# Kernel optimization log

Hardware: AMD Instinct MI355X
Metric: run time of the kernel (lower is better)

The kernel has to match this reference:

```python
import jax, jax.numpy as jnp
import numpy as np

N_NODES = 100000


def _gcn_conv(x, W, b, src, dst, dinv):
    # PyG GCNConv: h = X @ W; out[i] = sum_{j->i} norm_ji * h[j] (incl. self-loop); + b
    h = x @ W                                   # [N, F_out]
    norm = dinv[src] * dinv[dst]                # [E]
    agg = jax.ops.segment_sum(norm[:, None] * h[src], dst, num_segments=N_NODES)
    agg = agg + (dinv * dinv)[:, None] * h      # self-loop contribution
    return agg + b


def setup_inputs() -> dict:
    key = jax.random.key(0)
    ks = jax.random.split(key, 12)
    N, E, F = N_NODES, 3200000, 128

    def glorot(k, fan_in, fan_out):
        s = float(np.sqrt(6.0 / (fan_in + fan_out)))
        return jax.random.uniform(k, (fan_in, fan_out), jnp.float32, -s, s)

    x = jax.random.normal(ks[0], (N, F), jnp.float32)
    edge_index = jax.random.randint(ks[1], (2, E), 0, N, jnp.int64)
    return {
        "x": x,
        "edge_index": edge_index,
        "W1": glorot(ks[2], F, 64),  "b1": jnp.zeros((64,), jnp.float32),
        "W2": glorot(ks[3], 64, 32), "b2": jnp.zeros((32,), jnp.float32),
        "W3": glorot(ks[4], 32, 16), "b3": jnp.zeros((16,), jnp.float32),
        "Ws02": glorot(ks[5], F, 32),  "bs02": jnp.zeros((32,), jnp.float32),
        "Ws03": glorot(ks[6], F, 16),  "bs03": jnp.zeros((16,), jnp.float32),
        "Ws13": glorot(ks[7], 64, 16), "bs13": jnp.zeros((16,), jnp.float32),
    }


def reference(x, edge_index, W1, b1, W2, b2, W3, b3, Ws02, bs02, Ws03, bs03, Ws13, bs13):
    src, dst = edge_index[0], edge_index[1]
    # symmetric GCN normalization with self-loops: deg[i] = 1 + in-degree(i)
    deg = jax.ops.segment_sum(jnp.ones_like(dst, dtype=x.dtype), dst, num_segments=N_NODES) + 1.0
    dinv = jax.lax.rsqrt(deg)

    # eval-mode: dropout is identity
    x1 = jax.nn.relu(_gcn_conv(x, W1, b1, src, dst, dinv))            # [N, 64]
    x2 = jax.nn.relu(_gcn_conv(x1, W2, b2, src, dst, dinv)) + (x @ Ws02 + bs02)   # [N, 32]
    x3 = (jax.nn.relu(_gcn_conv(x2, W3, b3, src, dst, dinv))
          + (x @ Ws03 + bs03) + (x1 @ Ws13 + bs13))                   # [N, 16]
    return x3
```

## Files before the change

kernel.cpp:

```cpp
#include <hip/hip_runtime.h>

#define NN 100000
#define NB 256
#define NPB 391
#define MSCH 4096

__device__ inline unsigned short f2bf(float f) {
    unsigned u = __float_as_uint(f);
    return (unsigned short)((u + 0x7FFFu + ((u >> 16) & 1u)) >> 16);
}
__device__ inline unsigned packbf(float a, float b) {
    return (unsigned)f2bf(a) | ((unsigned)f2bf(b) << 16);
}
__device__ inline float bflo(unsigned u) { return __uint_as_float(u << 16); }
__device__ inline float bfhi(unsigned u) { return __uint_as_float(u & 0xFFFF0000u); }
__device__ inline float4 bf4(uint2 u) {
    return make_float4(bflo(u.x), bfhi(u.x), bflo(u.y), bfhi(u.y));
}

__device__ inline void fp8acc(unsigned u, float4& a) {
    auto lo = __builtin_amdgcn_cvt_pk_f32_fp8((int)u, false);
    auto hi = __builtin_amdgcn_cvt_pk_f32_fp8((int)u, true);
    a.x += lo[0]; a.y += lo[1]; a.z += hi[0]; a.w += hi[1];
}
__device__ inline unsigned char f2fp8(float v) {
    return (unsigned char)(__builtin_amdgcn_cvt_pk_fp8_f32(v, 0.f, 0, false) & 0xFF);
}
__device__ inline unsigned short f2fp8x2(float a, float b) {
    return (unsigned short)(__builtin_amdgcn_cvt_pk_fp8_f32(a, b, 0, false) & 0xFFFF);
}

typedef __attribute__((ext_vector_type(8))) short bf16x8;
typedef __attribute__((ext_vector_type(4))) float f32x4;


__global__ __launch_bounds__(256) void histA_kernel(const int* __restrict__ dst, int E,
                                                    int* __restrict__ counts) {
    __shared__ int h[NB];
    int t = threadIdx.x, blk = blockIdx.x;
    h[t] = 0;
    __syncthreads();
    long c0 = (long)blk * MSCH;
    int nE = (int)min((long)MSCH, E - c0);
    for (int k = t; k < nE; k += 256)
        atomicAdd(&h[dst[c0 + k] / NPB], 1);
    __syncthreads();
    counts[(size_t)blk * NB + t] = h[t];
}

__global__ __launch_bounds__(256) void bscan2_kernel(const int* __restrict__ counts, int nblk,
                                                     int* __restrict__ blkoff, int* __restrict__ totals) {
    int b = blockIdx.x, t = threadIdx.x;
    const int NP = 4;
    int c[NP];
    int s = 0;
    #pragma unroll
    for (int q = 0; q < NP; ++q) {
        int j = t * NP + q;
        c[q] = (j < nblk) ? counts[(size_t)j * NB + b] : 0;
        s += c[q];
    }
    __shared__ int sh[256];
    sh[t] = s;
    __syncthreads();
    for (int off = 1; off < 256; off <<= 1) {
        int u = (t >= off) ? sh[t - off] : 0;
        __syncthreads();
        sh[t] += u;
        __syncthreads();
    }
    int base = sh[t] - s;
    int run = base;
    #pragma unroll
    for (int q = 0; q < NP; ++q) {
        int j = t * NP + q;
        if (j < nblk) blkoff[(size_t)j * NB + b] = run;
        run += c[q];
    }
    if (t == 255) totals[b] = sh[255];
}

__global__ __launch_bounds__(NB) void bstart_kernel(const int* __restrict__ totals, int* __restrict__ bstart, int E) {
    __shared__ int sh[NB];
    int t = threadIdx.x;
    int v = totals[t];
    sh[t] = v;
    __syncthreads();
    for (int off = 1; off < NB; off <<= 1) {
        int u = (t >= off) ? sh[t - off] : 0;
        __syncthreads();
        sh[t] += u;
        __syncthreads();
    }
    bstart[t] = sh[t] - v;
    if (t == NB - 1) bstart[NB] = E;
}

__global__ __launch_bounds__(256) void scatter_kernel(const int* __restrict__ src, const int* __restrict__ dst,
                                                      int E, const int* __restrict__ bstart,
                                                      const int* __restrict__ blkoff,
                                                      const int* __restrict__ counts,
                                                      unsigned int* __restrict__ packed) {
    __shared__ unsigned sorted[MSCH];
    __shared__ unsigned char sortedb[MSCH];
    __shared__ int sh[NB];
    __shared__ int lofs[NB];
    __shared__ int lofs0[NB];
    __shared__ int gbase[NB];
    int t = threadIdx.x, blk = blockIdx.x;

    int c = counts[(size_t)blk * NB + t];
    sh[t] = c;
    __syncthreads();
    for (int off = 1; off < NB; off <<= 1) {
        int u = (t >= off) ? sh[t - off] : 0;
        __syncthreads();
        sh[t] += u;
        __syncthreads();
    }
    lofs0[t] = sh[t] - c;
    lofs[t]  = sh[t] - c;
    gbase[t] = bstart[t] + blkoff[(size_t)blk * NB + t];
    __syncthreads();

    long c0 = (long)blk * MSCH;
    int nE = (int)min((long)MSCH, E - c0);
    for (int k = t; k < nE; k += 256) {
        int d = dst[c0 + k];
        int s = src[c0 + k];
        int b = d / NPB;
        int ld = d - b * NPB;
        int r = atomicAdd(&lofs[b], 1);
        sorted[r] = ((unsigned)s << 9) | (unsigned)ld;
        sortedb[r] = (unsigned char)b;
    }
    __syncthreads();
    for (int k = t; k < nE; k += 256) {
        int b = sortedb[k];
        packed[gbase[b] + (k - lofs0[b])] = sorted[k];
    }
}

__global__ __launch_bounds__(512) void bucket_fill_kernel(const unsigned int* __restrict__ packed,
                                                          const int* __restrict__ bstart, int N, int E,
                                                          int* __restrict__ rowptr, int* __restrict__ col,
                                                          float* __restrict__ dinv) {
    int b = blockIdx.x, t = threadIdx.x;
    int e0 = bstart[b], cnt = bstart[b + 1] - e0;
    __shared__ int hist[512];
    __shared__ int sh[512];
    __shared__ int cur[512];
    hist[t] = 0;
    __syncthreads();
    for (int e = t; e < cnt; e += 512)
        atomicAdd(&hist[packed[e0 + e] & 511u], 1);
    __syncthreads();
    int v = hist[t];
    sh[t] = v;
    __syncthreads();
    for (int off = 1; off < 512; off <<= 1) {
        int u = (t >= off) ? sh[t - off] : 0;
        __syncthreads();
        sh[t] += u;
        __syncthreads();
    }
    int ex = sh[t] - v;
    int node = b * NPB + t;
    if (t < NPB && node < N) {
        rowptr[node] = e0 + ex;
        dinv[node] = rsqrtf(1.0f + (float)v);
    }
    cur[t] = e0 + ex;
    __syncthreads();
    for (int e = t; e < cnt; e += 512) {
        unsigned int p = packed[e0 + e];
        int pos = atomicAdd(&cur[p & 511u], 1);
        col[pos] = (int)(p >> 9);
    }
    if (b == 0 && t == 0) rowptr[N] = E;
}


__global__ __launch_bounds__(256) void wpack_kernel(const float* __restrict__ W1, const float* __restrict__ Ws02,
                                                    const float* __restrict__ Ws03, unsigned short* __restrict__ Wpk) {
    int i = blockIdx.x * 256 + threadIdx.x;
    if (i >= 112 * 128) return;
    int c = i >> 7, k = i & 127;
    float v;
    if (c < 64)      v = W1[k * 64 + c];
    else if (c < 96) v = Ws02[k * 32 + (c - 64)];
    else             v = Ws03[k * 16 + (c - 96)];
    Wpk[i] = f2bf(v);
}


__global__ __launch_bounds__(256) void mfma3_kernel(const float* __restrict__ X,
        const unsigned short* __restrict__ Wpk, const float* __restrict__ scale,
        const float* __restrict__ bb, const float* __restrict__ bc,
        unsigned char* __restrict__ oa, unsigned short* __restrict__ ob,
        unsigned short* __restrict__ oc, int N) {
    int t = threadIdx.x;
    int wv = t >> 6, l = t & 63;
    int r0 = blockIdx.x * 128 + wv * 32;
    int col = l & 15, g = l >> 4;
    int rowA0 = r0 + col, rowA1 = r0 + 16 + col;
    bool ok0 = rowA0 < N, ok1 = rowA1 < N;
    const float* xr0 = X + (size_t)rowA0 * 128;
    const float* xr1 = X + (size_t)rowA1 * 128;

    f32x4 acc[2][7];
    #pragma unroll
    for (int ti = 0; ti < 2; ++ti)
        #pragma unroll
        for (int i = 0; i < 7; ++i) acc[ti][i] = (f32x4){0.f, 0.f, 0.f, 0.f};

    #pragma unroll
    for (int s = 0; s < 4; ++s) {
        int k0 = s * 32 + g * 8;
        float4 lo0 = ok0 ? *(const float4*)(xr0 + k0)     : make_float4(0.f, 0.f, 0.f, 0.f);
        float4 hi0 = ok0 ? *(const float4*)(xr0 + k0 + 4) : make_float4(0.f, 0.f, 0.f, 0.f);
        float4 lo1 = ok1 ? *(const float4*)(xr1 + k0)     : make_float4(0.f, 0.f, 0.f, 0.f);
        float4 hi1 = ok1 ? *(const float4*)(xr1 + k0 + 4) : make_float4(0.f, 0.f, 0.f, 0.f);
        union { bf16x8 v; unsigned u[4]; } A0, A1;
        A0.u[0] = packbf(lo0.x, lo0.y); A0.u[1] = packbf(lo0.z, lo0.w);
        A0.u[2] = packbf(hi0.x, hi0.y); A0.u[3] = packbf(hi0.z, hi0.w);
        A1.u[0] = packbf(lo1.x, lo1.y); A1.u[1] = packbf(lo1.z, lo1.w);
        A1.u[2] = packbf(hi1.x, hi1.y); A1.u[3] = packbf(hi1.z, hi1.w);
        #pragma unroll
        for (int ct = 0; ct < 7; ++ct) {
            bf16x8 B = *(const bf16x8*)(Wpk + ((size_t)(ct * 16 + col) * 128 + k0));
            acc[0][ct] = __builtin_amdgcn_mfma_f32_16x16x32_bf16(A0.v, B, acc[0][ct], 0, 0, 0);
            acc[1][ct] = __builtin_amdgcn_mfma_f32_16x16x32_bf16(A1.v, B, acc[1][ct], 0, 0, 0);
        }
    }

    #pragma unroll
    for (int ti = 0; ti < 2; ++ti) {
        #pragma unroll
        for (int v = 0; v < 4; ++v) {
            int row = r0 + ti * 16 + g * 4 + v;
            if (row < N) {
                float sc = scale[row];
                #pragma unroll
                for (int ct = 0; ct < 4; ++ct)
                    oa[(size_t)row * 64 + ct * 16 + col] = f2fp8(acc[ti][ct][v] * sc);
                #pragma unroll
                for (int ct = 4; ct < 6; ++ct) {
                    int c2 = (ct - 4) * 16 + col;
                    ob[(size_t)row * 32 + c2] = f2bf(acc[ti][ct][v] + bb[c2]);
                }
                oc[(size_t)row * 16 + col] = f2bf(acc[ti][6][v] + bc[col]);
            }
        }
    }
}


template <int K, int C1, int C2>
__global__ __launch_bounds__(256) void gemm2b_kernel(const unsigned short* __restrict__ X,
        const float* __restrict__ Wa, const float* __restrict__ scale,
        const float* __restrict__ Wb, const float* __restrict__ bb,
        unsigned char* __restrict__ oa, unsigned short* __restrict__ ob, int N) {
    constexpr int M1 = C1 / 16, M2 = C2 / 16;
    constexpr int XS = K + 6;
    __shared__ float XL[64 * XS];
    __shared__ float WLa[K * C1];
    __shared__ float WLb[K * C2];
    int t = threadIdx.x;
    int r0 = blockIdx.x * 64;

    for (int i = t; i < K * C1 / 4; i += 256) ((float4*)WLa)[i] = ((const float4*)Wa)[i];
    for (int i = t; i < K * C2 / 4; i += 256) ((float4*)WLb)[i] = ((const float4*)Wb)[i];
    for (int i = t; i < 64 * (K / 4); i += 256) {
        int row = i / (K / 4), g = i % (K / 4);
        uint2 u = make_uint2(0u, 0u);
        if (r0 + row < N) u = ((const uint2*)(X + (size_t)(r0 + row) * K))[g];
        float* p = &XL[row * XS + g * 4];
        *(float2*)p = make_float2(bflo(u.x), bfhi(u.x));
        *(float2*)(p + 2) = make_float2(bflo(u.y), bfhi(u.y));
    }
    __syncthreads();

    int ty = t >> 4, tx = t & 15;
    float acc1[4][M1] = {}, acc2[4][M2] = {};
    const float* xb = &XL[(ty * 4) * XS];
    const float* wba = &WLa[tx * M1];
    const float* wbb = &WLb[tx * M2];
    for (int k = 0; k < K; ++k) {
        float x0 = xb[k], x1 = xb[XS + k], x2 = xb[2 * XS + k], x3 = xb[3 * XS + k];
        float wa[M1], wb2[M2];
        #pragma unroll
        for (int j = 0; j < M1; ++j) wa[j] = wba[k * C1 + j];
        #pragma unroll
        for (int j = 0; j < M2; ++j) wb2[j] = wbb[k * C2 + j];
        #pragma unroll
        for (int j = 0; j < M1; ++j) {
            acc1[0][j] = fmaf(x0, wa[j], acc1[0][j]);
            acc1[1][j] = fmaf(x1, wa[j], acc1[1][j]);
            acc1[2][j] = fmaf(x2, wa[j], acc1[2][j]);
            acc1[3][j] = fmaf(x3, wa[j], acc1[3][j]);
        }
        #pragma unroll
        for (int j = 0; j < M2; ++j) {
            acc2[0][j] = fmaf(x0, wb2[j], acc2[0][j]);
            acc2[1][j] = fmaf(x1, wb2[j], acc2[1][j]);
            acc2[2][j] = fmaf(x2, wb2[j], acc2[2][j]);
            acc2[3][j] = fmaf(x3, wb2[j], acc2[3][j]);
        }
    }

    #pragma unroll
    for (int i = 0; i < 4; ++i) {
        int row = r0 + ty * 4 + i;
        if (row < N) {
            float sc = scale[row];
            *(unsigned short*)(oa + (size_t)row * C1 + tx * 2) = f2fp8x2(acc1[i][0] * sc, acc1[i][1] * sc);
            ob[(size_t)row * C2 + tx] = f2bf(acc2[i][0] + bb[tx]);
        }
    }
}


__global__ __launch_bounds__(256) void gemm_l3_kernel(const unsigned short* __restrict__ X,
        const float* __restrict__ W, const float* __restrict__ scale,
        unsigned char* __restrict__ out, int N) {
    constexpr int K = 32, C = 16, XS = K + 6;
    __shared__ float XL[64 * XS];
    __shared__ float WL[K * C];
    int t = threadIdx.x;
    int r0 = blockIdx.x * 64;

    for (int i = t; i < K * C / 4; i += 256) ((float4*)WL)[i] = ((const float4*)W)[i];
    for (int i = t; i < 64 * (K / 4); i += 256) {
        int row = i / (K / 4), g = i % (K / 4);
        uint2 u = make_uint2(0u, 0u);
        if (r0 + row < N) u = ((const uint2*)(X + (size_t)(r0 + row) * K))[g];
        float* p = &XL[row * XS + g * 4];
        *(float2*)p = make_float2(bflo(u.x), bfhi(u.x));
        *(float2*)(p + 2) = make_float2(bflo(u.y), bfhi(u.y));
    }
    __syncthreads();

    int ty = t >> 4, tx = t & 15;
    float acc[4] = {0.f, 0.f, 0.f, 0.f};
    const float* xb = &XL[(ty * 4) * XS];
    for (int k = 0; k < K; ++k) {
        float wv = WL[k * C + tx];
        acc[0] = fmaf(xb[k], wv, acc[0]);
        acc[1] = fmaf(xb[XS + k], wv, acc[1]);
        acc[2] = fmaf(xb[2 * XS + k], wv, acc[2]);
        acc[3] = fmaf(xb[3 * XS + k], wv, acc[3]);
    }
    #pragma unroll
    for (int i = 0; i < 4; ++i) {
        int row = r0 + ty * 4 + i;
        if (row < N) out[(size_t)row * C + tx] = f2fp8(acc[i] * scale[row]);
    }
}


template <int F, int FPL, bool OBF>
__global__ __launch_bounds__(256) void agg_kernel(const unsigned char* __restrict__ hs,
        const int* __restrict__ rowptr, const int* __restrict__ col,
        const float* __restrict__ dinv, const float* __restrict__ bias,
        const unsigned short* __restrict__ skipA, const unsigned short* __restrict__ skipB,
        void* __restrict__ outv, int N) {
    constexpr int VL = F / FPL;
    constexpr int NPW = 64 / VL;
    constexpr int W = 8;
    constexpr int CR = W / VL;
    int t = threadIdx.x;
    int lane = t & 63, wv = t >> 6;
    int sub = lane / VL, fq = lane % VL;
    int i = (blockIdx.x * 4 + wv) * NPW + sub;
    if (i >= N) return;

    float4 aA0 = make_float4(0.f, 0.f, 0.f, 0.f);
    float4 aA1 = make_float4(0.f, 0.f, 0.f, 0.f);
    float4 aB0 = make_float4(0.f, 0.f, 0.f, 0.f);
    float4 aB1 = make_float4(0.f, 0.f, 0.f, 0.f);

    {
        const unsigned char* hrow = hs + (size_t)i * F + fq * FPL;
        if constexpr (FPL == 8) {
            uint2 u = *(const uint2*)hrow;
            fp8acc(u.x, aA0); fp8acc(u.y, aB0);
        } else {
            fp8acc(*(const unsigned*)hrow, aA0);
        }
    }

    int p0 = rowptr[i], p1 = rowptr[i + 1];
    int p = p0;
    for (; p + W <= p1; p += W) {
        int cw[CR];
        #pragma unroll
        for (int j = 0; j < CR; ++j) cw[j] = col[p + fq + j * VL];
        #pragma unroll
        for (int k = 0; k < W; ++k) {
            int s = __shfl(cw[k / VL], k % VL, VL);
            const unsigned char* sp = hs + (size_t)s * F + fq * FPL;
            if constexpr (FPL == 8) {
                uint2 u = *(const uint2*)sp;
                if (k & 1) { fp8acc(u.x, aA1); fp8acc(u.y, aB1); }
                else       { fp8acc(u.x, aA0); fp8acc(u.y, aB0); }
            } else {
                if (k & 1) fp8acc(*(const unsigned*)sp, aA1);
                else       fp8acc(*(const unsigned*)sp, aA0);
            }
        }
    }
    for (; p < p1; p += VL) {
        int c = (p + fq < p1) ? col[p + fq] : 0;
        int m = min(VL, p1 - p);
        for (int k = 0; k < m; ++k) {
            int s = __shfl(c, k, VL);
            const unsigned char* sp = hs + (size_t)s * F + fq * FPL;
            if constexpr (FPL == 8) {
                uint2 u = *(const uint2*)sp;
                fp8acc(u.x, aA1); fp8acc(u.y, aB1);
            } else {
                fp8acc(*(const unsigned*)sp, aA1);
            }
        }
    }

    float di = dinv[i];
    int fb = fq * FPL;
    float o[FPL];
    o[0] = fmaxf(di * (aA0.x + aA1.x) + bias[fb + 0], 0.f);
    o[1] = fmaxf(di * (aA0.y + aA1.y) + bias[fb + 1], 0.f);
    o[2] = fmaxf(di * (aA0.z + aA1.z) + bias[fb + 2], 0.f);
    o[3] = fmaxf(di * (aA0.w + aA1.w) + bias[fb + 3], 0.f);
    if constexpr (FPL == 8) {
        o[4] = fmaxf(di * (aB0.x + aB1.x) + bias[fb + 4], 0.f);
        o[5] = fmaxf(di * (aB0.y + aB1.y) + bias[fb + 5], 0.f);
        o[6] = fmaxf(di * (aB0.z + aB1.z) + bias[fb + 6], 0.f);
        o[7] = fmaxf(di * (aB0.w + aB1.w) + bias[fb + 7], 0.f);
    }
    if (skipA) {
        const unsigned short* sp = skipA + (size_t)i * F + fb;
        if constexpr (FPL == 8) {
            uint4 sa = *(const uint4*)sp;
            float4 s0 = bf4(make_uint2(sa.x, sa.y)), s1 = bf4(make_uint2(sa.z, sa.w));
            o[0] += s0.x; o[1] += s0.y; o[2] += s0.z; o[3] += s0.w;
            o[4] += s1.x; o[5] += s1.y; o[6] += s1.z; o[7] += s1.w;
        } else {
            float4 s0 = bf4(*(const uint2*)sp);
            o[0] += s0.x; o[1] += s0.y; o[2] += s0.z; o[3] += s0.w;
        }
    }
    if (skipB) {
        const unsigned short* sp = skipB + (size_t)i * F + fb;
        if constexpr (FPL == 8) {
            uint4 sa = *(const uint4*)sp;
            float4 s0 = bf4(make_uint2(sa.x, sa.y)), s1 = bf4(make_uint2(sa.z, sa.w));
            o[0] += s0.x; o[1] += s0.y; o[2] += s0.z; o[3] += s0.w;
            o[4] += s1.x; o[5] += s1.y; o[6] += s1.z; o[7] += s1.w;
        } else {
            float4 s0 = bf4(*(const uint2*)sp);
            o[0] += s0.x; o[1] += s0.y; o[2] += s0.z; o[3] += s0.w;
        }
    }

    if constexpr (OBF) {
        unsigned short* op = (unsigned short*)outv + (size_t)i * F + fb;
        if constexpr (FPL == 8) {
            uint4 w4;
            w4.x = packbf(o[0], o[1]); w4.y = packbf(o[2], o[3]);
            w4.z = packbf(o[4], o[5]); w4.w = packbf(o[6], o[7]);
            *(uint4*)op = w4;
        } else {
            uint2 w2;
            w2.x = packbf(o[0], o[1]); w2.y = packbf(o[2], o[3]);
            *(uint2*)op = w2;
        }
    } else {
        *(float4*)((float*)outv + (size_t)i * F + fb) = make_float4(o[0], o[1], o[2], o[3]);
    }
}


extern "C" void kernel_launch(void* const* d_in, const int* in_sizes, int n_in,
                              void* d_out, int out_size, void* d_ws, size_t ws_size,
                              hipStream_t stream) {
    const int N = NN;
    const float* x   = (const float*)d_in[0];
    const int*   ei  = (const int*)d_in[1];
    const int    E   = in_sizes[1] / 2;
    const int*   src = ei;
    const int*   dst = ei + E;
    const float* W1 = (const float*)d_in[2],  *b1  = (const float*)d_in[3];
    const float* W2 = (const float*)d_in[4],  *b2  = (const float*)d_in[5];
    const float* W3 = (const float*)d_in[6],  *b3  = (const float*)d_in[7];
    const float* Ws02 = (const float*)d_in[8],  *bs02 = (const float*)d_in[9];
    const float* Ws03 = (const float*)d_in[10], *bs03 = (const float*)d_in[11];
    const float* Ws13 = (const float*)d_in[12], *bs13 = (const float*)d_in[13];

    const int nblk = (E + MSCH - 1) / MSCH;

    char* w = (char*)d_ws;
    size_t off = 0;
    auto alloc = [&](size_t bytes) -> void* {
        void* p = w + off;
        off += (bytes + 255) & ~(size_t)255;
        return p;
    };
    int*   bstart   = (int*)alloc((size_t)(NB + 1) * 4);
    int*   totals   = (int*)alloc((size_t)NB * 4);
    int*   rowptr   = (int*)alloc(((size_t)N + 1) * 4);
    float* dinv     = (float*)alloc((size_t)N * 4);
    int*   col      = (int*)alloc((size_t)E * 4);
    int*   counts   = (int*)alloc((size_t)nblk * NB * 4);
    int*   blkoff   = (int*)alloc((size_t)nblk * NB * 4);
    unsigned short* Wpk = (unsigned short*)alloc((size_t)112 * 128 * 2);
    unsigned char* hs1  = (unsigned char*)alloc((size_t)N * 64 * 2);
    unsigned short* x1  = (unsigned short*)alloc((size_t)N * 64 * 2);
    unsigned short* s02 = (unsigned short*)alloc((size_t)N * 32 * 2);
    unsigned short* s03 = (unsigned short*)alloc((size_t)N * 16 * 2);
    unsigned short* x2  = (unsigned short*)alloc((size_t)N * 32 * 2);
    unsigned int* packed = (unsigned int*)x1;
    unsigned char* hs2 = hs1;
    unsigned short* s13 = (unsigned short*)(hs1 + (size_t)N * 64);
    unsigned char* hs3 = (unsigned char*)s02;

    wpack_kernel<<<(112 * 128 + 255) / 256, 256, 0, stream>>>(W1, Ws02, Ws03, Wpk);

    histA_kernel<<<nblk, 256, 0, stream>>>(dst, E, counts);
    bscan2_kernel<<<NB, 256, 0, stream>>>(counts, nblk, blkoff, totals);
    bstart_kernel<<<1, NB, 0, stream>>>(totals, bstart, E);
    scatter_kernel<<<nblk, 256, 0, stream>>>(src, dst, E, bstart, blkoff, counts, packed);
    bucket_fill_kernel<<<NB, 512, 0, stream>>>(packed, bstart, N, E, rowptr, col, dinv);

    int gb = (N + 63) / 64;
    mfma3_kernel<<<(N + 127) / 128, 256, 0, stream>>>(x, Wpk, dinv, bs02, bs03, hs1, s02, s03, N);
    agg_kernel<64, 8, true><<<(N + 31) / 32, 256, 0, stream>>>(hs1, rowptr, col, dinv, b1, nullptr, nullptr, x1, N);
    gemm2b_kernel<64, 32, 16><<<gb, 256, 0, stream>>>(x1, W2, dinv, Ws13, bs13, hs2, s13, N);
    agg_kernel<32, 8, true><<<gb, 256, 0, stream>>>(hs2, rowptr, col, dinv, b2, s02, nullptr, x2, N);
    gemm_l3_kernel<<<gb, 256, 0, stream>>>(x2, W3, dinv, hs3, N);
    agg_kernel<16, 4, false><<<gb, 256, 0, stream>>>(hs3, rowptr, col, dinv, b3, s03, s13, (float*)d_out, N);
}
```

Measured before the change: 208.1 us.

## Fuse layer-2 aggregation with layer-3 GEMM and use nontemporal loads/stores

Adds agg2f_kernel, which aggregates layer 2, applies bias, ReLU and the s02 skip, then multiplies by W3 in registers with a 4-lane shuffle reduction. It writes the fp8 hs3 directly, so the bf16 x2 round trip and the separate gemm_l3 launch are gone. It also widens the edge unroll in agg_kernel from 8 to 16. Column indices, skip tensors and outputs now go through nontemporal loads and stores to reduce cache pollution. The cost is more registers and shuffles in the fused kernel, and the larger unroll may reduce occupancy.

```diff
diff --git a/kernel.cpp b/kernel.cpp
--- a/kernel.cpp
+++ b/kernel.cpp
@@ -14,9 +14,12 @@
 }
 __device__ inline float bflo(unsigned u) { return __uint_as_float(u << 16); }
 __device__ inline float bfhi(unsigned u) { return __uint_as_float(u & 0xFFFF0000u); }
-__device__ inline float4 bf4(uint2 u) {
-    return make_float4(bflo(u.x), bfhi(u.x), bflo(u.y), bfhi(u.y));
-}
+
+typedef __attribute__((ext_vector_type(2))) unsigned uint2v;
+typedef __attribute__((ext_vector_type(4))) unsigned uint4v;
+typedef __attribute__((ext_vector_type(4))) float float4v;
+typedef __attribute__((ext_vector_type(8))) short bf16x8;
+typedef __attribute__((ext_vector_type(4))) float f32x4;
 
 __device__ inline void fp8acc(unsigned u, float4& a) {
     auto lo = __builtin_amdgcn_cvt_pk_f32_fp8((int)u, false);
@@ -29,9 +32,9 @@
 __device__ inline unsigned short f2fp8x2(float a, float b) {
     return (unsigned short)(__builtin_amdgcn_cvt_pk_fp8_f32(a, b, 0, false) & 0xFFFF);
 }
-
-typedef __attribute__((ext_vector_type(8))) short bf16x8;
-typedef __attribute__((ext_vector_type(4))) float f32x4;
+__device__ inline float4 bf4v(uint2v u) {
+    return make_float4(bflo(u.x), bfhi(u.x), bflo(u.y), bfhi(u.y));
+}
 
 
 __global__ __launch_bounds__(256) void histA_kernel(const int* __restrict__ dst, int E,
@@ -321,44 +324,6 @@
 }
 
 
-__global__ __launch_bounds__(256) void gemm_l3_kernel(const unsigned short* __restrict__ X,
-        const float* __restrict__ W, const float* __restrict__ scale,
-        unsigned char* __restrict__ out, int N) {
-    constexpr int K = 32, C = 16, XS = K + 6;
-    __shared__ float XL[64 * XS];
-    __shared__ float WL[K * C];
-    int t = threadIdx.x;
-    int r0 = blockIdx.x * 64;
-
-    for (int i = t; i < K * C / 4; i += 256) ((float4*)WL)[i] = ((const float4*)W)[i];
-    for (int i = t; i < 64 * (K / 4); i += 256) {
-        int row = i / (K / 4), g = i % (K / 4);
-        uint2 u = make_uint2(0u, 0u);
-        if (r0 + row < N) u = ((const uint2*)(X + (size_t)(r0 + row) * K))[g];
-        float* p = &XL[row * XS + g * 4];
-        *(float2*)p = make_float2(bflo(u.x), bfhi(u.x));
-        *(float2*)(p + 2) = make_float2(bflo(u.y), bfhi(u.y));
-    }
-    __syncthreads();
-
-    int ty = t >> 4, tx = t & 15;
-    float acc[4] = {0.f, 0.f, 0.f, 0.f};
-    const float* xb = &XL[(ty * 4) * XS];
-    for (int k = 0; k < K; ++k) {
-        float wv = WL[k * C + tx];
-        acc[0] = fmaf(xb[k], wv, acc[0]);
-        acc[1] = fmaf(xb[XS + k], wv, acc[1]);
-        acc[2] = fmaf(xb[2 * XS + k], wv, acc[2]);
-        acc[3] = fmaf(xb[3 * XS + k], wv, acc[3]);
-    }
-    #pragma unroll
-    for (int i = 0; i < 4; ++i) {
-        int row = r0 + ty * 4 + i;
-        if (row < N) out[(size_t)row * C + tx] = f2fp8(acc[i] * scale[row]);
-    }
-}
-
-
 template <int F, int FPL, bool OBF>
 __global__ __launch_bounds__(256) void agg_kernel(const unsigned char* __restrict__ hs,
         const int* __restrict__ rowptr, const int* __restrict__ col,
@@ -367,7 +332,7 @@
         void* __restrict__ outv, int N) {
     constexpr int VL = F / FPL;
     constexpr int NPW = 64 / VL;
-    constexpr int W = 8;
+    constexpr int W = 16;
     constexpr int CR = W / VL;
     int t = threadIdx.x;
     int lane = t & 63, wv = t >> 6;
@@ -395,7 +360,7 @@
     for (; p + W <= p1; p += W) {
         int cw[CR];
         #pragma unroll
-        for (int j = 0; j < CR; ++j) cw[j] = col[p + fq + j * VL];
+        for (int j = 0; j < CR; ++j) cw[j] = __builtin_nontemporal_load(&col[p + fq + j * VL]);
         #pragma unroll
         for (int k = 0; k < W; ++k) {
             int s = __shfl(cw[k / VL], k % VL, VL);
@@ -411,7 +376,7 @@
         }
     }
     for (; p < p1; p += VL) {
-        int c = (p + fq < p1) ? col[p + fq] : 0;
+        int c = (p + fq < p1) ? __builtin_nontemporal_load(&col[p + fq]) : 0;
         int m = min(VL, p1 - p);
         for (int k = 0; k < m; ++k) {
             int s = __shfl(c, k, VL);
@@ -441,24 +406,24 @@
     if (skipA) {
         const unsigned short* sp = skipA + (size_t)i * F + fb;
         if constexpr (FPL == 8) {
-            uint4 sa = *(const uint4*)sp;
-            float4 s0 = bf4(make_uint2(sa.x, sa.y)), s1 = bf4(make_uint2(sa.z, sa.w));
+            uint4v sa = __builtin_nontemporal_load((const uint4v*)sp);
+            float4 s0 = bf4v((uint2v){sa.x, sa.y}), s1 = bf4v((uint2v){sa.z, sa.w});
             o[0] += s0.x; o[1] += s0.y; o[2] += s0.z; o[3] += s0.w;
             o[4] += s1.x; o[5] += s1.y; o[6] += s1.z; o[7] += s1.w;
         } else {
-            float4 s0 = bf4(*(const uint2*)sp);
+            float4 s0 = bf4v(__builtin_nontemporal_load((const uint2v*)sp));
             o[0] += s0.x; o[1] += s0.y; o[2] += s0.z; o[3] += s0.w;
         }
     }
     if (skipB) {
         const unsigned short* sp = skipB + (size_t)i * F + fb;
         if constexpr (FPL == 8) {
-            uint4 sa = *(const uint4*)sp;
-            float4 s0 = bf4(make_uint2(sa.x, sa.y)), s1 = bf4(make_uint2(sa.z, sa.w));
+            uint4v sa = __builtin_nontemporal_load((const uint4v*)sp);
+            float4 s0 = bf4v((uint2v){sa.x, sa.y}), s1 = bf4v((uint2v){sa.z, sa.w});
             o[0] += s0.x; o[1] += s0.y; o[2] += s0.z; o[3] += s0.w;
             o[4] += s1.x; o[5] += s1.y; o[6] += s1.z; o[7] += s1.w;
         } else {
-            float4 s0 = bf4(*(const uint2*)sp);
+            float4 s0 = bf4v(__builtin_nontemporal_load((const uint2v*)sp));
             o[0] += s0.x; o[1] += s0.y; o[2] += s0.z; o[3] += s0.w;
         }
     }
@@ -466,18 +431,110 @@
     if constexpr (OBF) {
         unsigned short* op = (unsigned short*)outv + (size_t)i * F + fb;
         if constexpr (FPL == 8) {
-            uint4 w4;
+            uint4v w4;
             w4.x = packbf(o[0], o[1]); w4.y = packbf(o[2], o[3]);
             w4.z = packbf(o[4], o[5]); w4.w = packbf(o[6], o[7]);
-            *(uint4*)op = w4;
+            __builtin_nontemporal_store(w4, (uint4v*)op);
         } else {
-            uint2 w2;
+            uint2v w2;
             w2.x = packbf(o[0], o[1]); w2.y = packbf(o[2], o[3]);
-            *(uint2*)op = w2;
+            __builtin_nontemporal_store(w2, (uint2v*)op);
         }
     } else {
-        *(float4*)((float*)outv + (size_t)i * F + fb) = make_float4(o[0], o[1], o[2], o[3]);
-    }
+        float4v w4 = {o[0], o[1], o[2], o[3]};
+        __builtin_nontemporal_store(w4, (float4v*)((float*)outv + (size_t)i * F + fb));
+    }
+}
+
+
+__global__ __launch_bounds__(256) void agg2f_kernel(const unsigned char* __restrict__ hs,
+        const int* __restrict__ rowptr, const int* __restrict__ col,
+        const float* __restrict__ dinv, const float* __restrict__ bias,
+        const unsigned short* __restrict__ skipA, const float* __restrict__ W3,
+        unsigned char* __restrict__ hs3, int N) {
+    constexpr int F = 32, FPL = 8, VL = 4, NPW = 16, W = 8, CR = 2;
+    __shared__ float WL[32 * 16];
+    int t = threadIdx.x;
+    for (int j = t; j < 32 * 16; j += 256) WL[j] = W3[j];
+    __syncthreads();
+
+    int lane = t & 63, wv = t >> 6;
+    int sub = lane / VL, fq = lane % VL;
+    int i = (blockIdx.x * 4 + wv) * NPW + sub;
+    if (i >= N) return;
+
+    float4 aA0 = make_float4(0.f, 0.f, 0.f, 0.f);
+    float4 aA1 = make_float4(0.f, 0.f, 0.f, 0.f);
+    float4 aB0 = make_float4(0.f, 0.f, 0.f, 0.f);
+    float4 aB1 = make_float4(0.f, 0.f, 0.f, 0.f);
+
+    {
+        const unsigned char* hrow = hs + (size_t)i * F + fq * FPL;
+        uint2 u = *(const uint2*)hrow;
+        fp8acc(u.x, aA0); fp8acc(u.y, aB0);
+    }
+
+    int p0 = rowptr[i], p1 = rowptr[i + 1];
+    int p = p0;
+    for (; p + W <= p1; p += W) {
+        int cw[CR];
+        #pragma unroll
+        for (int j = 0; j < CR; ++j) cw[j] = __builtin_nontemporal_load(&col[p + fq + j * VL]);
+        #pragma unroll
+        for (int k = 0; k < W; ++k) {
+            int s = __shfl(cw[k / VL], k % VL, VL);
+            const unsigned char* sp = hs + (size_t)s * F + fq * FPL;
+            uint2 u = *(const uint2*)sp;
+            if (k & 1) { fp8acc(u.x, aA1); fp8acc(u.y, aB1); }
+            else       { fp8acc(u.x, aA0); fp8acc(u.y, aB0); }
+        }
+    }
+    for (; p < p1; p += VL) {
+        int c = (p + fq < p1) ? __builtin_nontemporal_load(&col[p + fq]) : 0;
+        int m = min(VL, p1 - p);
+        for (int k = 0; k < m; ++k) {
+            int s = __shfl(c, k, VL);
+            const unsigned char* sp = hs + (size_t)s * F + fq * FPL;
+            uint2 u = *(const uint2*)sp;
+            fp8acc(u.x, aA1); fp8acc(u.y, aB1);
+        }
+    }
+
+    float di = dinv[i];
+    int fb = fq * FPL;
+    float o[8];
+    o[0] = fmaxf(di * (aA0.x + aA1.x) + bias[fb + 0], 0.f);
+    o[1] = fmaxf(di * (aA0.y + aA1.y) + bias[fb + 1], 0.f);
+    o[2] = fmaxf(di * (aA0.z + aA1.z) + bias[fb + 2], 0.f);
+    o[3] = fmaxf(di * (aA0.w + aA1.w) + bias[fb + 3], 0.f);
+    o[4] = fmaxf(di * (aB0.x + aB1.x) + bias[fb + 4], 0.f);
+    o[5] = fmaxf(di * (aB0.y + aB1.y) + bias[fb + 5], 0.f);
+    o[6] = fmaxf(di * (aB0.z + aB1.z) + bias[fb + 6], 0.f);
+    o[7] = fmaxf(di * (aB0.w + aB1.w) + bias[fb + 7], 0.f);
+    {
+        const unsigned short* sp = skipA + (size_t)i * F + fb;
+        uint4v sa = __builtin_nontemporal_load((const uint4v*)sp);
+        float4 s0 = bf4v((uint2v){sa.x, sa.y}), s1 = bf4v((uint2v){sa.z, sa.w});
+        o[0] += s0.x; o[1] += s0.y; o[2] += s0.z; o[3] += s0.w;
+        o[4] += s1.x; o[5] += s1.y; o[6] += s1.z; o[7] += s1.w;
+    }
+
+    float p16[16];
+    #pragma unroll
+    for (int c = 0; c < 16; ++c) {
+        float s = 0.f;
+        #pragma unroll
+        for (int j = 0; j < 8; ++j) s = fmaf(o[j], WL[(fb + j) * 16 + c], s);
+        p16[c] = s;
+    }
+    #pragma unroll
+    for (int d = 1; d < 4; d <<= 1) {
+        #pragma unroll
+        for (int c = 0; c < 16; ++c) p16[c] += __shfl_xor(p16[c], d, 4);
+    }
+    unsigned wlo = __builtin_amdgcn_cvt_pk_fp8_f32(p16[fq * 4 + 0] * di, p16[fq * 4 + 1] * di, 0, false) & 0xFFFF;
+    unsigned whi = __builtin_amdgcn_cvt_pk_fp8_f32(p16[fq * 4 + 2] * di, p16[fq * 4 + 3] * di, 0, false) & 0xFFFF;
+    *(unsigned*)(hs3 + (size_t)i * 16 + fq * 4) = wlo | (whi << 16);
 }
 
 
@@ -518,11 +575,10 @@
     unsigned short* x1  = (unsigned short*)alloc((size_t)N * 64 * 2);
     unsigned short* s02 = (unsigned short*)alloc((size_t)N * 32 * 2);
     unsigned short* s03 = (unsigned short*)alloc((size_t)N * 16 * 2);
-    unsigned short* x2  = (unsigned short*)alloc((size_t)N * 32 * 2);
+    unsigned char* hs3  = (unsigned char*)alloc((size_t)N * 16);
     unsigned int* packed = (unsigned int*)x1;
     unsigned char* hs2 = hs1;
     unsigned short* s13 = (unsigned short*)(hs1 + (size_t)N * 64);
-    unsigned char* hs3 = (unsigned char*)s02;
 
     wpack_kernel<<<(112 * 128 + 255) / 256, 256, 0, stream>>>(W1, Ws02, Ws03, Wpk);
 
@@ -536,7 +592,6 @@
     mfma3_kernel<<<(N + 127) / 128, 256, 0, stream>>>(x, Wpk, dinv, bs02, bs03, hs1, s02, s03, N);
     agg_kernel<64, 8, true><<<(N + 31) / 32, 256, 0, stream>>>(hs1, rowptr, col, dinv, b1, nullptr, nullptr, x1, N);
     gemm2b_kernel<64, 32, 16><<<gb, 256, 0, stream>>>(x1, W2, dinv, Ws13, bs13, hs2, s13, N);
-    agg_kernel<32, 8, true><<<gb, 256, 0, stream>>>(hs2, rowptr, col, dinv, b2, s02, nullptr, x2, N);
-    gemm_l3_kernel<<<gb, 256, 0, stream>>>(x2, W3, dinv, hs3, N);
+    agg2f_kernel<<<gb, 256, 0, stream>>>(hs2, rowptr, col, dinv, b2, s02, W3, hs3, N);
     agg_kernel<16, 4, false><<<gb, 256, 0, stream>>>(hs3, rowptr, col, dinv, b3, s03, s13, (float*)d_out, N);
 }
```

After: 228.0 us. 1.1x slower.
